# Optimization experiments

Hardware: AMD Instinct MI355X
Metric: run time of the kernel (lower is better)

The kernel has to match this reference:

```python
import jax, jax.numpy as jnp
import numpy as np

VOCAB = 5000
EMB = 256
RNN = 512
FEAT = 512
L = 400
B = 32
T = 150  # max_generate_steps - 1
ATT = 512


def setup_inputs() -> dict:
    key = jax.random.key(0)
    ks = jax.random.split(key, 12)
    s = lambda k, *sh: jax.random.normal(k, sh, dtype=jnp.float32) * 0.05
    return {
        "features": jax.random.normal(ks[0], (B, L, FEAT), dtype=jnp.float32),
        "init_state": jnp.zeros((B, RNN), dtype=jnp.float32),
        "emb": s(ks[1], VOCAB, EMB),
        "gru_kernel": s(ks[2], EMB + RNN, 3 * RNN),
        "gru_rec_kernel": s(ks[3], RNN, 3 * RNN),
        "gru_bias": jnp.zeros((2, 3 * RNN), dtype=jnp.float32),
        "attn_W1": s(ks[4], FEAT, ATT),
        "attn_W2": s(ks[5], RNN, ATT),
        "attn_V": s(ks[6], ATT, 1),
        "out_W": s(ks[7], RNN + FEAT, RNN),
        "proj_W": s(ks[8], RNN, VOCAB),
        "formula": jax.random.randint(ks[9], (B, T), 0, VOCAB),
    }


def _decode(features, init_state, emb, gru_kernel, gru_rec_kernel, gru_bias,
            attn_W1, attn_W2, attn_V, out_W, proj_W, formula):
    # Precompute W1(features): same math as recomputing per step.  [B, L, ATT]
    feat_proj = jnp.einsum("blf,fa->bla", features, attn_W1)

    def step(carry, tok):
        state, last_out = carry  # [B, RNN], [B, RNN]
        x = emb[tok]  # [B, EMB]
        inp = jnp.concatenate([x, last_out], axis=-1)  # [B, EMB+RNN]
        # Keras GRU (reset_after=True), gate order z, r, h
        mx = inp @ gru_kernel + gru_bias[0]
        mh = state @ gru_rec_kernel + gru_bias[1]
        xz, xr, xh = jnp.split(mx, 3, axis=-1)
        rz, rr, rh = jnp.split(mh, 3, axis=-1)
        z = jax.nn.sigmoid(xz + rz)
        r = jax.nn.sigmoid(xr + rr)
        hh = jnp.tanh(xh + r * rh)
        h = z * state + (1.0 - z) * hh  # [B, RNN]
        # Bahdanau attention
        score = jnp.tanh(feat_proj + (h @ attn_W2)[:, None, :]) @ attn_V  # [B, L, 1]
        w = jax.nn.softmax(score, axis=1)
        ctx = jnp.sum(w * features, axis=1)  # [B, FEAT]
        out_state = jnp.tanh(jnp.concatenate([h, ctx], axis=-1) @ out_W)  # [B, RNN]
        logits = out_state @ proj_W  # [B, VOCAB]
        return (h, out_state), logits

    carry0 = (init_state, jnp.zeros_like(init_state))
    toks = formula.T  # [T, B]
    _, logits = jax.lax.scan(step, carry0, toks)
    return jnp.transpose(logits, (1, 0, 2))  # [B, T, VOCAB]


def reference(features, init_state, emb, gru_kernel, gru_rec_kernel, gru_bias,
              attn_W1, attn_W2, attn_V, out_W, proj_W, formula):
    return _decode(features, init_state, emb, gru_kernel, gru_rec_kernel, gru_bias,
                   attn_W1, attn_W2, attn_V, out_W, proj_W, formula)
```

## Files before the change

kernel.cpp:

```cpp
#include <hip/hip_runtime.h>

#define BB 32
#define TT 150
#define LL 400
#define FEATD 512
#define RNND 512
#define ATTD 512
#define EMBD 256
#define VOCABD 5000
#define G3 1536

__device__ __forceinline__ float fsigmoid(float x) { return 1.f / (1.f + __expf(-x)); }
__device__ __forceinline__ float ftanh(float x) {
    x = fminf(15.f, fmaxf(-15.f, x));
    float e = __expf(2.f * x);
    return 1.f - 2.f / (e + 1.f);
}
__device__ __forceinline__ void fma4(float4& a, const float4 w, const float s) {
    a.x += w.x * s; a.y += w.y * s; a.z += w.z * s; a.w += w.w * s;
}

__global__ void __launch_bounds__(256) k_proj512(const float* __restrict__ features,
                                                 const float* __restrict__ W,
                                                 float* __restrict__ outb) {
    __shared__ float sa[64 * 68];
    int blt = blockIdx.x >> 2, at = blockIdx.x & 3;
    int bl0 = blt * 64;
    int tid = threadIdx.x;
    int aq = tid & 31, blg = tid >> 5;
    float4 acc[8] = {};
    for (int kc = 0; kc < FEATD; kc += 64) {
        __syncthreads();
        for (int it = 0; it < 16; ++it) {
            int lin = it * 256 + tid;
            int k = lin & 63, bl = lin >> 6;
            sa[k * 68 + bl] = features[((size_t)bl0 + bl) * FEATD + kc + k];
        }
        __syncthreads();
#pragma unroll 4
        for (int k = 0; k < 64; ++k) {
            float4 w = *(const float4*)&W[(size_t)(kc + k) * 512 + at * 128 + aq * 4];
            float4 s0 = *(const float4*)&sa[k * 68 + blg * 8];
            float4 s1 = *(const float4*)&sa[k * 68 + blg * 8 + 4];
            fma4(acc[0], w, s0.x); fma4(acc[1], w, s0.y);
            fma4(acc[2], w, s0.z); fma4(acc[3], w, s0.w);
            fma4(acc[4], w, s1.x); fma4(acc[5], w, s1.y);
            fma4(acc[6], w, s1.z); fma4(acc[7], w, s1.w);
        }
    }
#pragma unroll
    for (int i = 0; i < 8; ++i)
        *(float4*)&outb[((size_t)bl0 + blg * 8 + i) * 512 + at * 128 + aq * 4] = acc[i];
}

__global__ void __launch_bounds__(512) k_gates(
    const float* __restrict__ emb, const int* __restrict__ formula,
    const float* __restrict__ Wk, const float* __restrict__ Wr,
    const float* __restrict__ hin, const float* __restrict__ hppT,
    const float* __restrict__ gdotT, const float* __restrict__ esumT,
    float* __restrict__ mxp, float* __restrict__ mhp,
    float* __restrict__ los, int t) {
    __shared__ float sm[256 * 33];
    __shared__ float sinv[BB];
    __shared__ int stok[BB];
    int id = blockIdx.x, tid = threadIdx.x;
    bool isMX = id < 72;
    int jt, ks; const float* W; float* ob;
    if (isMX) { jt = id / 3; ks = id % 3; W = Wk; ob = mxp; }
    else { int r = id - 72; jt = r >> 1; ks = r & 1; W = Wr; ob = mhp; }
    int k0 = ks * 256;
    if (isMX && ks == 0 && tid < BB) stok[tid] = formula[tid * TT + t];
    if (isMX && ks > 0 && t > 0 && tid < BB) {
        float4 e0 = *(const float4*)&esumT[tid * 8];
        float4 e1 = *(const float4*)&esumT[tid * 8 + 4];
        sinv[tid] = 1.f / (e0.x + e0.y + e0.z + e0.w + e1.x + e1.y + e1.z + e1.w);
    }
    __syncthreads();
    for (int it = 0; it < 16; ++it) {
        int lin = it * 512 + tid;
        int k = lin & 255, b = lin >> 8;
        float v;
        if (!isMX) {
            v = hin[(size_t)b * RNND + k0 + k];
        } else if (ks == 0) {
            v = emb[(size_t)stok[b] * EMBD + k];
        } else {
            int kr = (ks - 1) * 256 + k;
            if (t == 0) {
                v = 0.f;
            } else {
                float4 hp = *(const float4*)&hppT[((size_t)b * RNND + kr) * 4];
                float4 g0 = *(const float4*)&gdotT[((size_t)b * RNND + kr) * 8];
                float4 g1 = *(const float4*)&gdotT[((size_t)b * RNND + kr) * 8 + 4];
                float hps = hp.x + hp.y + hp.z + hp.w;
                float gg = g0.x + g0.y + g0.z + g0.w + g1.x + g1.y + g1.z + g1.w;
                v = ftanh(hps + sinv[b] * gg);
            }
            if (jt == 0) los[((size_t)t * BB + b) * RNND + kr] = v;
        }
        sm[k * 33 + b] = v;
    }
    __syncthreads();
    int jq = tid & 15, b = tid >> 4;
    int j = jt * 64 + jq * 4;
    float4 acc = {0, 0, 0, 0};
#pragma unroll 4
    for (int k = 0; k < 256; ++k) {
        float4 w = *(const float4*)&W[(size_t)(k0 + k) * G3 + j];
        fma4(acc, w, sm[k * 33 + b]);
    }
    *(float4*)&ob[((size_t)ks * BB + b) * G3 + j] = acc;
}

__global__ void __launch_bounds__(512) k_qh(
    const float* __restrict__ mxp, const float* __restrict__ mhp,
    const float* __restrict__ gruB, const float* __restrict__ W2,
    const float* __restrict__ outW, const float* __restrict__ hin,
    float* __restrict__ hout, float* __restrict__ qpT,
    float* __restrict__ hppT) {
    __shared__ float sm[128 * 33];
    int tile = blockIdx.x >> 2, ks = blockIdx.x & 3;
    int tid = threadIdx.x;
    int k0 = ks * 128;
    for (int it = 0; it < 8; ++it) {
        int lin = it * 512 + tid;
        int k = lin & 127, b = lin >> 7;
        int j = k0 + k;
        size_t m0 = ((size_t)0 * BB + b) * G3, m1 = ((size_t)1 * BB + b) * G3,
               m2 = ((size_t)2 * BB + b) * G3;
        float xz = gruB[j] + mxp[m0 + j] + mxp[m1 + j] + mxp[m2 + j];
        float xr = gruB[512 + j] + mxp[m0 + 512 + j] + mxp[m1 + 512 + j] + mxp[m2 + 512 + j];
        float xh = gruB[1024 + j] + mxp[m0 + 1024 + j] + mxp[m1 + 1024 + j] + mxp[m2 + 1024 + j];
        float rz = gruB[G3 + j] + mhp[m0 + j] + mhp[m1 + j];
        float rr = gruB[G3 + 512 + j] + mhp[m0 + 512 + j] + mhp[m1 + 512 + j];
        float rh = gruB[G3 + 1024 + j] + mhp[m0 + 1024 + j] + mhp[m1 + 1024 + j];
        float z = fsigmoid(xz + rz), r = fsigmoid(xr + rr);
        float hh = ftanh(xh + r * rh);
        float hn = z * hin[(size_t)b * RNND + j] + (1.f - z) * hh;
        sm[k * 33 + b] = hn;
        if (tile == 0) hout[(size_t)b * RNND + j] = hn;
    }
    __syncthreads();
    const float* W = (tile < 8) ? W2 : outW;
    int cb = (tile & 7) * 64;
    int jq = tid & 15, b = tid >> 4;
    int j = cb + jq * 4;
    float4 acc = {0, 0, 0, 0};
#pragma unroll 4
    for (int k = 0; k < 128; ++k) {
        float4 w = *(const float4*)&W[(size_t)(k0 + k) * 512 + j];
        fma4(acc, w, sm[k * 33 + b]);
    }
    float* outp = (tile < 8) ? qpT : hppT;
    float av[4] = {acc.x, acc.y, acc.z, acc.w};
#pragma unroll
    for (int i = 0; i < 4; ++i)
        outp[((size_t)b * 512 + j + i) * 4 + ks] = av[i];
}

__global__ void __launch_bounds__(512) k_attn(
    const float* __restrict__ qpT, const float* __restrict__ V,
    const float* __restrict__ fp, const float* __restrict__ G,
    float* __restrict__ gdotT, float* __restrict__ esumT) {
    __shared__ float sq[ATTD];
    __shared__ float sV[ATTD];
    __shared__ float se[64];
    int b = blockIdx.x >> 3, ls = blockIdx.x & 7, l0 = ls * 50;
    int tid = threadIdx.x;
    {
        float4 qp = *(const float4*)&qpT[((size_t)b * 512 + tid) * 4];
        sq[tid] = qp.x + qp.y + qp.z + qp.w;
        sV[tid] = V[tid];
    }
    if (tid >= 50 && tid < 64) se[tid] = 0.f;
    __syncthreads();
    int lane = tid & 63, wv = tid >> 6;
    float4 q0 = ((const float4*)sq)[lane], q1 = ((const float4*)sq)[64 + lane];
    float4 v0 = ((const float4*)sV)[lane], v1 = ((const float4*)sV)[64 + lane];
    for (int ll = wv; ll < 50; ll += 8) {
        const float4* row = (const float4*)(fp + ((size_t)b * LL + l0 + ll) * ATTD);
        float4 f0 = row[lane], f1 = row[64 + lane];
        float d = ftanh(f0.x + q0.x) * v0.x + ftanh(f0.y + q0.y) * v0.y +
                  ftanh(f0.z + q0.z) * v0.z + ftanh(f0.w + q0.w) * v0.w +
                  ftanh(f1.x + q1.x) * v1.x + ftanh(f1.y + q1.y) * v1.y +
                  ftanh(f1.z + q1.z) * v1.z + ftanh(f1.w + q1.w) * v1.w;
#pragma unroll
        for (int o = 32; o > 0; o >>= 1) d += __shfl_xor(d, o);
        if (lane == 0) se[ll] = __expf(d);
    }
    __syncthreads();
    if (tid < 64) {
        float x = se[tid];
#pragma unroll
        for (int o = 32; o > 0; o >>= 1) x += __shfl_xor(x, o);
        if (tid == 0) esumT[b * 8 + ls] = x;
    }
    float a = 0.f;
#pragma unroll 2
    for (int l = 0; l < 50; ++l)
        a += se[l] * G[((size_t)b * LL + l0 + l) * RNND + tid];
    gdotT[((size_t)b * RNND + tid) * 8 + ls] = a;
}

__global__ void __launch_bounds__(512) k_lo_tail(
    const float* __restrict__ hppT, const float* __restrict__ gdotT,
    const float* __restrict__ esumT, float* __restrict__ los) {
    int b = blockIdx.x, tid = threadIdx.x;
    float4 e0 = *(const float4*)&esumT[b * 8];
    float4 e1 = *(const float4*)&esumT[b * 8 + 4];
    float inv = 1.f / (e0.x + e0.y + e0.z + e0.w + e1.x + e1.y + e1.z + e1.w);
    float4 hp = *(const float4*)&hppT[((size_t)b * RNND + tid) * 4];
    float4 g0 = *(const float4*)&gdotT[((size_t)b * RNND + tid) * 8];
    float4 g1 = *(const float4*)&gdotT[((size_t)b * RNND + tid) * 8 + 4];
    float hps = hp.x + hp.y + hp.z + hp.w;
    float gg = g0.x + g0.y + g0.z + g0.w + g1.x + g1.y + g1.z + g1.w;
    los[((size_t)TT * BB + b) * RNND + tid] = ftanh(hps + inv * gg);
}

__global__ void __launch_bounds__(256) k_final(
    const float* __restrict__ los, const float* __restrict__ Wp,
    float* __restrict__ out) {
    __shared__ float sa[64 * 68];
    __shared__ unsigned srow[64];
    int mt = blockIdx.x / 40, vt = blockIdx.x % 40;
    int r0 = mt * 64;
    int tid = threadIdx.x;
    if (tid < 64) {
        int r = r0 + tid;
        int bb = r / TT, t = r % TT;
        srow[tid] = (unsigned)(((size_t)(t + 1) * BB + bb) * RNND);
    }
    int aq = tid & 31, blg = tid >> 5;
    int v = vt * 128 + aq * 4;
    bool vok = v < VOCABD;
    float4 acc[8] = {};
    __syncthreads();
    for (int kc = 0; kc < RNND; kc += 64) {
        for (int it = 0; it < 16; ++it) {
            int lin = it * 256 + tid;
            int k = lin & 63, rl = lin >> 6;
            sa[k * 68 + rl] = los[srow[rl] + kc + k];
        }
        __syncthreads();
        if (vok) {
#pragma unroll 4
            for (int k = 0; k < 64; ++k) {
                float4 w = *(const float4*)&Wp[(size_t)(kc + k) * VOCABD + v];
                float4 s0 = *(const float4*)&sa[k * 68 + blg * 8];
                float4 s1 = *(const float4*)&sa[k * 68 + blg * 8 + 4];
                fma4(acc[0], w, s0.x); fma4(acc[1], w, s0.y);
                fma4(acc[2], w, s0.z); fma4(acc[3], w, s0.w);
                fma4(acc[4], w, s1.x); fma4(acc[5], w, s1.y);
                fma4(acc[6], w, s1.z); fma4(acc[7], w, s1.w);
            }
        }
        __syncthreads();
    }
    if (vok) {
#pragma unroll
        for (int i = 0; i < 8; ++i)
            *(float4*)&out[(size_t)(r0 + blg * 8 + i) * VOCABD + v] = acc[i];
    }
}

extern "C" void kernel_launch(void* const* d_in, const int* in_sizes, int n_in,
                              void* d_out, int out_size, void* d_ws, size_t ws_size,
                              hipStream_t stream) {
    const float* features  = (const float*)d_in[0];
    const float* initstate = (const float*)d_in[1];
    const float* emb       = (const float*)d_in[2];
    const float* gruK      = (const float*)d_in[3];
    const float* gruR      = (const float*)d_in[4];
    const float* gruB      = (const float*)d_in[5];
    const float* W1        = (const float*)d_in[6];
    const float* W2        = (const float*)d_in[7];
    const float* V         = (const float*)d_in[8];
    const float* outW      = (const float*)d_in[9];
    const float* projW     = (const float*)d_in[10];
    const int*   formula   = (const int*)d_in[11];
    float* logits = (float*)d_out;

    float* ws = (float*)d_ws;
    float* h0    = ws;
    float* h1    = h0 + (size_t)BB * RNND;
    float* mxp   = h1 + (size_t)BB * RNND;
    float* mhp   = mxp + (size_t)3 * BB * G3;
    float* qpT   = mhp + (size_t)2 * BB * G3;
    float* hppT  = qpT + (size_t)BB * 512 * 4;
    float* gdotT = hppT + (size_t)BB * 512 * 4;
    float* esumT = gdotT + (size_t)BB * RNND * 8;
    float* los   = esumT + BB * 8;
    float* fp    = los + (size_t)(TT + 1) * BB * RNND;
    float* G     = fp + (size_t)BB * LL * ATTD;

    hipMemsetAsync(los, 0, (size_t)BB * RNND * sizeof(float), stream);
    hipMemcpyAsync(h0, initstate, (size_t)BB * RNND * sizeof(float),
                   hipMemcpyDeviceToDevice, stream);

    k_proj512<<<800, 256, 0, stream>>>(features, W1, fp);
    k_proj512<<<800, 256, 0, stream>>>(features, outW + (size_t)512 * RNND, G);

    float* hin = h0;
    float* hout = h1;
    for (int t = 0; t < TT; ++t) {
        k_gates<<<120, 512, 0, stream>>>(emb, formula, gruK, gruR, hin,
                                         hppT, gdotT, esumT, mxp, mhp, los, t);
        k_qh<<<64, 512, 0, stream>>>(mxp, mhp, gruB, W2, outW, hin, hout,
                                     qpT, hppT);
        k_attn<<<256, 512, 0, stream>>>(qpT, V, fp, G, gdotT, esumT);
        float* tmp = hin; hin = hout; hout = tmp;
    }
    k_lo_tail<<<BB, 512, 0, stream>>>(hppT, gdotT, esumT, los);
    k_final<<<75 * 40, 256, 0, stream>>>(los, projW, logits);
}
```

Baseline: 10.48 ms.

## Fuse GRU update, query projection and attention into one per-step kernel

Merges the GRU-combine/projection kernel and the attention kernel into a single kernel launched per (batch, L-slice) block. Each block recomputes the new hidden state for its batch row, computes the full W2 query projection and a 64-column slice of the out_W hidden projection, then runs attention. This removes one launch per step and the split-K partial buffers, but each of the 8 blocks per batch row redundantly recomputes the 512x512 W2 GEMV, so the weight reads grow.

```diff
diff --git a/kernel.cpp b/kernel.cpp
--- a/kernel.cpp
+++ b/kernel.cpp
@@ -56,7 +56,7 @@
 __global__ void __launch_bounds__(512) k_gates(
     const float* __restrict__ emb, const int* __restrict__ formula,
     const float* __restrict__ Wk, const float* __restrict__ Wr,
-    const float* __restrict__ hin, const float* __restrict__ hppT,
+    const float* __restrict__ hin, const float* __restrict__ hpart,
     const float* __restrict__ gdotT, const float* __restrict__ esumT,
     float* __restrict__ mxp, float* __restrict__ mhp,
     float* __restrict__ los, int t) {
@@ -89,10 +89,9 @@
             if (t == 0) {
                 v = 0.f;
             } else {
-                float4 hp = *(const float4*)&hppT[((size_t)b * RNND + kr) * 4];
+                float hps = hpart[(size_t)b * RNND + kr];
                 float4 g0 = *(const float4*)&gdotT[((size_t)b * RNND + kr) * 8];
                 float4 g1 = *(const float4*)&gdotT[((size_t)b * RNND + kr) * 8 + 4];
-                float hps = hp.x + hp.y + hp.z + hp.w;
                 float gg = g0.x + g0.y + g0.z + g0.w + g1.x + g1.y + g1.z + g1.w;
                 v = ftanh(hps + sinv[b] * gg);
             }
@@ -112,20 +111,24 @@
     *(float4*)&ob[((size_t)ks * BB + b) * G3 + j] = acc;
 }
 
-__global__ void __launch_bounds__(512) k_qh(
+__global__ void __launch_bounds__(512) k_fused(
     const float* __restrict__ mxp, const float* __restrict__ mhp,
     const float* __restrict__ gruB, const float* __restrict__ W2,
-    const float* __restrict__ outW, const float* __restrict__ hin,
-    float* __restrict__ hout, float* __restrict__ qpT,
-    float* __restrict__ hppT) {
-    __shared__ float sm[128 * 33];
-    int tile = blockIdx.x >> 2, ks = blockIdx.x & 3;
+    const float* __restrict__ outW, const float* __restrict__ V,
+    const float* __restrict__ fp, const float* __restrict__ G,
+    const float* __restrict__ hin, float* __restrict__ hout,
+    float* __restrict__ hpart, float* __restrict__ gdotT,
+    float* __restrict__ esumT) {
+    __shared__ float sh[RNND];
+    __shared__ float sq[ATTD];
+    __shared__ float sV[ATTD];
+    __shared__ float se[64];
+    __shared__ float sred[512];
+    int b = blockIdx.x >> 3, ls = blockIdx.x & 7, l0 = ls * 50;
     int tid = threadIdx.x;
-    int k0 = ks * 128;
-    for (int it = 0; it < 8; ++it) {
-        int lin = it * 512 + tid;
-        int k = lin & 127, b = lin >> 7;
-        int j = k0 + k;
+
+    {
+        int j = tid;
         size_t m0 = ((size_t)0 * BB + b) * G3, m1 = ((size_t)1 * BB + b) * G3,
                m2 = ((size_t)2 * BB + b) * G3;
         float xz = gruB[j] + mxp[m0 + j] + mxp[m1 + j] + mxp[m2 + j];
@@ -137,43 +140,36 @@
         float z = fsigmoid(xz + rz), r = fsigmoid(xr + rr);
         float hh = ftanh(xh + r * rh);
         float hn = z * hin[(size_t)b * RNND + j] + (1.f - z) * hh;
-        sm[k * 33 + b] = hn;
-        if (tile == 0) hout[(size_t)b * RNND + j] = hn;
-    }
-    __syncthreads();
-    const float* W = (tile < 8) ? W2 : outW;
-    int cb = (tile & 7) * 64;
-    int jq = tid & 15, b = tid >> 4;
-    int j = cb + jq * 4;
-    float4 acc = {0, 0, 0, 0};
-#pragma unroll 4
-    for (int k = 0; k < 128; ++k) {
-        float4 w = *(const float4*)&W[(size_t)(k0 + k) * 512 + j];
-        fma4(acc, w, sm[k * 33 + b]);
-    }
-    float* outp = (tile < 8) ? qpT : hppT;
-    float av[4] = {acc.x, acc.y, acc.z, acc.w};
-#pragma unroll
-    for (int i = 0; i < 4; ++i)
-        outp[((size_t)b * 512 + j + i) * 4 + ks] = av[i];
-}
-
-__global__ void __launch_bounds__(512) k_attn(
-    const float* __restrict__ qpT, const float* __restrict__ V,
-    const float* __restrict__ fp, const float* __restrict__ G,
-    float* __restrict__ gdotT, float* __restrict__ esumT) {
-    __shared__ float sq[ATTD];
-    __shared__ float sV[ATTD];
-    __shared__ float se[64];
-    int b = blockIdx.x >> 3, ls = blockIdx.x & 7, l0 = ls * 50;
-    int tid = threadIdx.x;
+        sh[j] = hn;
+        if (ls == 0) hout[(size_t)b * RNND + j] = hn;
+        sV[j] = V[j];
+        if (j >= 50 && j < 64) se[j] = 0.f;
+    }
+    __syncthreads();
+
     {
-        float4 qp = *(const float4*)&qpT[((size_t)b * 512 + tid) * 4];
-        sq[tid] = qp.x + qp.y + qp.z + qp.w;
-        sV[tid] = V[tid];
-    }
-    if (tid >= 50 && tid < 64) se[tid] = 0.f;
-    __syncthreads();
+        float acc = 0.f;
+#pragma unroll 8
+        for (int k = 0; k < 512; ++k) acc += sh[k] * W2[(size_t)k * 512 + tid];
+        sq[tid] = acc;
+    }
+    {
+        int c = tid & 63, kq = tid >> 6;
+        int kb = kq * 64;
+        float acc = 0.f;
+#pragma unroll 8
+        for (int k = 0; k < 64; ++k)
+            acc += sh[kb + k] * outW[(size_t)(kb + k) * 512 + ls * 64 + c];
+        sred[tid] = acc;
+    }
+    __syncthreads();
+    if (tid < 64) {
+        float a = 0.f;
+#pragma unroll
+        for (int q2 = 0; q2 < 8; ++q2) a += sred[q2 * 64 + tid];
+        hpart[(size_t)b * RNND + ls * 64 + tid] = a;
+    }
+
     int lane = tid & 63, wv = tid >> 6;
     float4 q0 = ((const float4*)sq)[lane], q1 = ((const float4*)sq)[64 + lane];
     float4 v0 = ((const float4*)sV)[lane], v1 = ((const float4*)sV)[64 + lane];
@@ -195,6 +191,7 @@
         for (int o = 32; o > 0; o >>= 1) x += __shfl_xor(x, o);
         if (tid == 0) esumT[b * 8 + ls] = x;
     }
+
     float a = 0.f;
 #pragma unroll 2
     for (int l = 0; l < 50; ++l)
@@ -203,16 +200,15 @@
 }
 
 __global__ void __launch_bounds__(512) k_lo_tail(
-    const float* __restrict__ hppT, const float* __restrict__ gdotT,
+    const float* __restrict__ hpart, const float* __restrict__ gdotT,
     const float* __restrict__ esumT, float* __restrict__ los) {
     int b = blockIdx.x, tid = threadIdx.x;
     float4 e0 = *(const float4*)&esumT[b * 8];
     float4 e1 = *(const float4*)&esumT[b * 8 + 4];
     float inv = 1.f / (e0.x + e0.y + e0.z + e0.w + e1.x + e1.y + e1.z + e1.w);
-    float4 hp = *(const float4*)&hppT[((size_t)b * RNND + tid) * 4];
+    float hps = hpart[(size_t)b * RNND + tid];
     float4 g0 = *(const float4*)&gdotT[((size_t)b * RNND + tid) * 8];
     float4 g1 = *(const float4*)&gdotT[((size_t)b * RNND + tid) * 8 + 4];
-    float hps = hp.x + hp.y + hp.z + hp.w;
     float gg = g0.x + g0.y + g0.z + g0.w + g1.x + g1.y + g1.z + g1.w;
     los[((size_t)TT * BB + b) * RNND + tid] = ftanh(hps + inv * gg);
 }
@@ -285,9 +281,8 @@
     float* h1    = h0 + (size_t)BB * RNND;
     float* mxp   = h1 + (size_t)BB * RNND;
     float* mhp   = mxp + (size_t)3 * BB * G3;
-    float* qpT   = mhp + (size_t)2 * BB * G3;
-    float* hppT  = qpT + (size_t)BB * 512 * 4;
-    float* gdotT = hppT + (size_t)BB * 512 * 4;
+    float* hpart = mhp + (size_t)2 * BB * G3;
+    float* gdotT = hpart + (size_t)BB * RNND;
     float* esumT = gdotT + (size_t)BB * RNND * 8;
     float* los   = esumT + BB * 8;
     float* fp    = los + (size_t)(TT + 1) * BB * RNND;
@@ -304,12 +299,11 @@
     float* hout = h1;
     for (int t = 0; t < TT; ++t) {
         k_gates<<<120, 512, 0, stream>>>(emb, formula, gruK, gruR, hin,
-                                         hppT, gdotT, esumT, mxp, mhp, los, t);
-        k_qh<<<64, 512, 0, stream>>>(mxp, mhp, gruB, W2, outW, hin, hout,
-                                     qpT, hppT);
-        k_attn<<<256, 512, 0, stream>>>(qpT, V, fp, G, gdotT, esumT);
+                                         hpart, gdotT, esumT, mxp, mhp, los, t);
+        k_fused<<<256, 512, 0, stream>>>(mxp, mhp, gruB, W2, outW, V, fp, G,
+                                         hin, hout, hpart, gdotT, esumT);
         float* tmp = hin; hin = hout; hout = tmp;
     }
-    k_lo_tail<<<BB, 512, 0, stream>>>(hppT, gdotT, esumT, los);
+    k_lo_tail<<<BB, 512, 0, stream>>>(hpart, gdotT, esumT, los);
     k_final<<<75 * 40, 256, 0, stream>>>(los, projW, logits);
 }
```

Measured after the change: 12.06 ms. 1.15x slower.
